# Kernel tuning notes

Hardware: AMD Instinct MI355X
Metric: run time of the kernel (lower is better)

Reference implementation:

```python
import jax, jax.numpy as jnp
import numpy as np

VOCAB = 10000
HID = 1024
OUT = 10000
BATCH = 32
SEQ = 256


def setup_inputs() -> dict:
    key = jax.random.key(0)
    k1, k2, k3, k4 = jax.random.split(key, 4)
    inputs = jax.random.randint(k1, (BATCH, SEQ), 0, VOCAB, dtype=jnp.int32)
    state = jnp.zeros((BATCH, HID), dtype=jnp.float32)
    W_xh = 0.01 * jax.random.normal(k2, (VOCAB, HID), dtype=jnp.float32)
    W_hh = 0.01 * jax.random.normal(k3, (HID, HID), dtype=jnp.float32)
    W_hq = 0.01 * jax.random.normal(k4, (HID, OUT), dtype=jnp.float32)
    b_h = jnp.zeros((HID,), dtype=jnp.float32)
    b_q = jnp.zeros((OUT,), dtype=jnp.float32)
    return {"inputs": inputs, "state": state, "W_xh": W_xh, "W_hh": W_hh,
            "b_h": b_h, "W_hq": W_hq, "b_q": b_q}


def reference(inputs, state, W_xh, W_hh, b_h, W_hq, b_q):
    # inputs: (B, T) int ids. Original one-hots then matmuls with W_xh;
    # one_hot(x) @ W_xh == W_xh[x], so we use the gather form (same math).
    x_tb = inputs.T  # (T, B)

    def step(H, x_t):
        # x_t: (B,) ids; H: (B, HID)
        H = jnp.tanh(W_xh[x_t] + H @ W_hh + b_h)
        Y = H @ W_hq + b_q  # (B, OUT)
        return H, Y

    H_final, Ys = jax.lax.scan(step, state, x_tb)  # Ys: (T, B, OUT)
    # torch.cat(outputs, dim=0) over the time list -> (T*B, OUT)
    Y = Ys.reshape(-1, Ys.shape[-1])
    return Y, H_final
```

## Files before the change

### kernel.cpp

```cpp
#include <hip/hip_runtime.h>
#include <hip/hip_bf16.h>

#define VOCAB 10000
#define HID   1024
#define OUTN  10000
#define BATCH 32
#define SEQT  256
#define NPAD  10112

typedef short s16x8 __attribute__((ext_vector_type(8)));
typedef float f32x4 __attribute__((ext_vector_type(4)));
typedef unsigned u32x2 __attribute__((ext_vector_type(2)));

#define GLOAD_LDS16(gptr, lptr)                                                      \
  __builtin_amdgcn_global_load_lds((__attribute__((address_space(1))) void*)(gptr),  \
                                   (__attribute__((address_space(3))) void*)(lptr),  \
                                   16, 0, 0)

#define ALOAD16_SC(dst, base, off)                                                   \
  asm volatile("global_load_dwordx4 %0, %1, off offset:%2 sc0 sc1"                   \
               : "=v"(dst) : "v"(base), "n"(off) : "memory")

__device__ __forceinline__ unsigned bfbits(float f) {
  __hip_bfloat16 h = __float2bfloat16(f);
  return (unsigned)*reinterpret_cast<unsigned short*>(&h);
}

__global__ __launch_bounds__(256) void transpose_cast(
    const float* __restrict__ src, __hip_bfloat16* __restrict__ dst,
    int K, int N, int Npad) {
  __shared__ float tile[32][33];
  const int n0 = blockIdx.x * 32, k0 = blockIdx.y * 32;
  const int tx = threadIdx.x & 31, ty = threadIdx.x >> 5;
#pragma unroll
  for (int yy = 0; yy < 32; yy += 8) {
    const int k = k0 + ty + yy, n = n0 + tx;
    tile[ty + yy][tx] = (k < K && n < N) ? src[k * N + n] : 0.f;
  }
  __syncthreads();
#pragma unroll
  for (int yy = 0; yy < 32; yy += 8) {
    const int n = n0 + ty + yy, k = k0 + tx;
    if (n < Npad && k < K) dst[(size_t)n * K + k] = __float2bfloat16(tile[tx][ty + yy]);
  }
}

__global__ __launch_bounds__(256) void cast_state(
    const float* __restrict__ s, __hip_bfloat16* __restrict__ d, int n) {
  const int i = blockIdx.x * 256 + threadIdx.x;
  if (i < n) d[i] = __float2bfloat16(s[i]);
}

__global__ __launch_bounds__(256, 1) void rnn_persist(
    __hip_bfloat16* __restrict__ Hbf,
    const int* __restrict__ ids,
    const float* __restrict__ W_xh,
    const __hip_bfloat16* __restrict__ WhhT,
    const float* __restrict__ b_h,
    float* __restrict__ Hfin,
    unsigned* __restrict__ flags) {
  __shared__ __align__(16) __hip_bfloat16 whh[32 * HID];

  const int wg   = blockIdx.x;
  const int wave = threadIdx.x >> 6;
  const int lane = threadIdx.x & 63;
  const int wm = wave >> 1, wn = wave & 1;
  const int r0 = wm * 16;
  const int c0 = wg * 32 + wn * 16;
  const int l16 = lane & 15;
  const int g   = lane >> 4;

  for (int ci = threadIdx.x; ci < 32 * (HID / 8); ci += 256) {
    const int col = ci >> 7;
    const int c16 = ci & 127;
    const s16x8 v = *reinterpret_cast<const s16x8*>(
        WhhT + (size_t)(wg * 32 + col) * HID + c16 * 8);
    const int sw = (c16 & ~7) | ((c16 & 7) ^ (col & 7));
    *reinterpret_cast<s16x8*>(reinterpret_cast<char*>(whh) + col * 2048 + sw * 16) = v;
  }

  const int orow = r0 + l16;
  const int oc   = c0 + g * 4;
  const f32x4 bh4 = *reinterpret_cast<const f32x4*>(b_h + oc);

  f32x4 wxh4 = *reinterpret_cast<const f32x4*>(
      W_xh + (size_t)ids[orow * SEQT + 0] * HID + oc);

  __syncthreads();

  const int aOff = (r0 + l16) * HID + g * 8;
  const char* myB = reinterpret_cast<const char*>(whh) + (wn * 16 + l16) * 2048;
  const int xorv = l16 & 7;
  const int offE = (g ^ xorv) * 16;
  const int offO = ((g + 4) ^ xorv) * 16;

  for (int t = 0; t < SEQT; ++t) {
    const __hip_bfloat16* aBase = Hbf + (size_t)t * (BATCH * HID) + aOff;
    __hip_bfloat16* Hnext = Hbf + (size_t)(t + 1) * (BATCH * HID);

    s16x8 areg[32];
#pragma unroll
    for (int kk = 0; kk < 32; ++kk) ALOAD16_SC(areg[kk], aBase, kk * 64);
    asm volatile("s_waitcnt vmcnt(0)" ::: "memory");
    __builtin_amdgcn_sched_barrier(0);

    f32x4 acc0 = {0.f, 0.f, 0.f, 0.f}, acc1 = {0.f, 0.f, 0.f, 0.f};
#pragma unroll
    for (int kk = 0; kk < 32; kk += 2) {
      const s16x8 b0 = *reinterpret_cast<const s16x8*>(myB + (kk >> 1) * 128 + offE);
      const s16x8 b1 = *reinterpret_cast<const s16x8*>(myB + (kk >> 1) * 128 + offO);
      acc0 = __builtin_amdgcn_mfma_f32_16x16x32_bf16(b0, areg[kk],     acc0, 0, 0, 0);
      acc1 = __builtin_amdgcn_mfma_f32_16x16x32_bf16(b1, areg[kk + 1], acc1, 0, 0, 0);
    }

    float x[4];
#pragma unroll
    for (int jj = 0; jj < 4; ++jj) {
      const float s = acc0[jj] + acc1[jj] + wxh4[jj] + bh4[jj];
      const float e = __expf(2.f * s);
      x[jj] = 1.f - 2.f / (e + 1.f);
    }
    u32x2 pk;
    pk[0] = bfbits(x[0]) | (bfbits(x[1]) << 16);
    pk[1] = bfbits(x[2]) | (bfbits(x[3]) << 16);
    asm volatile("global_store_dwordx2 %0, %1, off sc0 sc1"
                 :: "v"(Hnext + orow * HID + oc), "v"(pk) : "memory");
    if (t == SEQT - 1)
      *reinterpret_cast<f32x4*>(Hfin + orow * HID + oc) = (f32x4){x[0], x[1], x[2], x[3]};

    if (t + 1 < SEQT) {
      asm volatile("s_waitcnt vmcnt(0)" ::: "memory");
      __syncthreads();
      if (threadIdx.x == 0) atomicExch(flags + wg * 32, (unsigned)(t + 1));

      wxh4 = *reinterpret_cast<const f32x4*>(
          W_xh + (size_t)ids[orow * SEQT + (t + 1)] * HID + oc);

      const unsigned* myflag = flags + (lane & 31) * 32;
      const unsigned target = (unsigned)(t + 1);
      unsigned f;
      do {
        asm volatile("global_load_dword %0, %1, off sc0 sc1\n\t"
                     "s_waitcnt vmcnt(0)"
                     : "=v"(f) : "v"(myflag) : "memory");
      } while (__all((int)(f >= target)) == 0);
      __builtin_amdgcn_sched_barrier(0);
    }
  }
}

__global__ __launch_bounds__(256) void gemm_out(
    const __hip_bfloat16* __restrict__ A,
    const __hip_bfloat16* __restrict__ BT,
    const float* __restrict__ b_q,
    float* __restrict__ Y) {
  __shared__ __align__(16) __hip_bfloat16 As[128 * 64];
  __shared__ __align__(16) __hip_bfloat16 Bs[128 * 64];

  const int bx = blockIdx.x;
  const int by = blockIdx.y;
  const int wave = threadIdx.x >> 6;
  const int lane = threadIdx.x & 63;
  const int wm = wave >> 1, wn = wave & 1;
  const int l16 = lane & 15;

  const size_t aRow0 = (size_t)by * 128;
  const size_t bRow0 = (size_t)bx * 128;

  f32x4 acc[4][4];
#pragma unroll
  for (int m = 0; m < 4; ++m)
#pragma unroll
    for (int n = 0; n < 4; ++n) acc[m][n] = (f32x4){0.f, 0.f, 0.f, 0.f};

  for (int kt = 0; kt < HID / 64; ++kt) {
    __syncthreads();
#pragma unroll
    for (int q = 0; q < 4; ++q) {
      const int ci = q * 256 + wave * 64 + lane;
      const int r  = ci >> 3;
      const int gc = (ci & 7) ^ (r & 7);
      const __hip_bfloat16* ga = A  + (aRow0 + r) * HID + kt * 64 + gc * 8;
      const __hip_bfloat16* gb = BT + (bRow0 + r) * HID + kt * 64 + gc * 8;
      GLOAD_LDS16(ga, &As[(q * 256 + wave * 64) * 8]);
      GLOAD_LDS16(gb, &Bs[(q * 256 + wave * 64) * 8]);
    }
    __syncthreads();

    s16x8 af[2][4], bf[2][4];
#pragma unroll
    for (int kc = 0; kc < 2; ++kc) {
      const int cc = kc * 4 + (lane >> 4);
#pragma unroll
      for (int m = 0; m < 4; ++m) {
        const int rowA = wm * 64 + m * 16 + l16;
        af[kc][m] = *reinterpret_cast<const s16x8*>(&As[rowA * 64 + ((cc ^ (rowA & 7)) * 8)]);
      }
#pragma unroll
      for (int n = 0; n < 4; ++n) {
        const int rowB = wn * 64 + n * 16 + l16;
        bf[kc][n] = *reinterpret_cast<const s16x8*>(&Bs[rowB * 64 + ((cc ^ (rowB & 7)) * 8)]);
      }
    }
#pragma unroll
    for (int kc = 0; kc < 2; ++kc)
#pragma unroll
      for (int m = 0; m < 4; ++m)
#pragma unroll
        for (int n = 0; n < 4; ++n)
          acc[m][n] = __builtin_amdgcn_mfma_f32_16x16x32_bf16(af[kc][m], bf[kc][n], acc[m][n], 0, 0, 0);
  }

  const int crow0 = by * 128 + wm * 64 + (lane >> 4) * 4;
  const int ccol0 = bx * 128 + wn * 64 + l16;
#pragma unroll
  for (int n = 0; n < 4; ++n) {
    const int ccol = ccol0 + n * 16;
    if (ccol < OUTN) {
      const float bq = b_q[ccol];
#pragma unroll
      for (int m = 0; m < 4; ++m) {
        const int crow = crow0 + m * 16;
#pragma unroll
        for (int j = 0; j < 4; ++j)
          Y[(size_t)(crow + j) * OUTN + ccol] = acc[m][n][j] + bq;
      }
    }
  }
}

extern "C" void kernel_launch(void* const* d_in, const int* in_sizes, int n_in,
                              void* d_out, int out_size, void* d_ws, size_t ws_size,
                              hipStream_t stream) {
  const int*   inputs = (const int*)d_in[0];
  const float* state  = (const float*)d_in[1];
  const float* W_xh   = (const float*)d_in[2];
  const float* W_hh   = (const float*)d_in[3];
  const float* b_h    = (const float*)d_in[4];
  const float* W_hq   = (const float*)d_in[5];
  const float* b_q    = (const float*)d_in[6];

  float* Y    = (float*)d_out;
  float* Hfin = Y + (size_t)SEQT * BATCH * OUTN;

  char* ws = (char*)d_ws;
  __hip_bfloat16* Hbf  = (__hip_bfloat16*)ws;
  __hip_bfloat16* WhhT = (__hip_bfloat16*)(ws + 16842752);
  __hip_bfloat16* WhqT = (__hip_bfloat16*)(ws + 16842752 + 2097152);
  unsigned* flags      = (unsigned*)(ws + 16842752 + 2097152 + 20709376 - 4096);

  transpose_cast<<<dim3(32, 32), 256, 0, stream>>>(W_hh, WhhT, HID, HID, HID);
  transpose_cast<<<dim3(NPAD / 32, 32), 256, 0, stream>>>(W_hq, WhqT, HID, OUTN, NPAD);
  cast_state<<<dim3(BATCH * HID / 256), 256, 0, stream>>>(state, Hbf, BATCH * HID);

  rnn_persist<<<dim3(32), dim3(256), 0, stream>>>(
      Hbf, inputs, W_xh, WhhT, b_h, Hfin, flags);

  gemm_out<<<dim3(NPAD / 128, 8192 / 128), 256, 0, stream>>>(Hbf + BATCH * HID, WhqT, b_q, Y);
}
```

Before: 1.764 ms.

## Fuse output projection into persistent RNN kernel via flag-synchronized consumer blocks

Adds consumer workgroups to the persistent recurrence kernel that wait on per-step mirror flags and compute Y for each timestep while the recurrence continues, replacing the separate output GEMM launch. Consumers read W_hq fragments straight from global memory without LDS staging. Flags are now zeroed each launch in the state-cast kernel. This risks extra memory traffic and polling contention slowing the latency-critical recurrence.

```diff
diff --git a/kernel.cpp b/kernel.cpp
--- a/kernel.cpp
+++ b/kernel.cpp
@@ -12,11 +12,6 @@
 typedef float f32x4 __attribute__((ext_vector_type(4)));
 typedef unsigned u32x2 __attribute__((ext_vector_type(2)));
 
-#define GLOAD_LDS16(gptr, lptr)                                                      \
-  __builtin_amdgcn_global_load_lds((__attribute__((address_space(1))) void*)(gptr),  \
-                                   (__attribute__((address_space(3))) void*)(lptr),  \
-                                   16, 0, 0)
-
 #define ALOAD16_SC(dst, base, off)                                                   \
   asm volatile("global_load_dwordx4 %0, %1, off offset:%2 sc0 sc1"                   \
                : "=v"(dst) : "v"(base), "n"(off) : "memory")
@@ -46,9 +41,11 @@
 }
 
 __global__ __launch_bounds__(256) void cast_state(
-    const float* __restrict__ s, __hip_bfloat16* __restrict__ d, int n) {
+    const float* __restrict__ s, __hip_bfloat16* __restrict__ d, int n,
+    unsigned* __restrict__ zero_base, int zero_n) {
   const int i = blockIdx.x * 256 + threadIdx.x;
   if (i < n) d[i] = __float2bfloat16(s[i]);
+  if (i < zero_n) zero_base[i] = 0u;
 }
 
 __global__ __launch_bounds__(256, 1) void rnn_persist(
@@ -58,172 +55,165 @@
     const __hip_bfloat16* __restrict__ WhhT,
     const float* __restrict__ b_h,
     float* __restrict__ Hfin,
-    unsigned* __restrict__ flags) {
-  __shared__ __align__(16) __hip_bfloat16 whh[32 * HID];
-
-  const int wg   = blockIdx.x;
-  const int wave = threadIdx.x >> 6;
-  const int lane = threadIdx.x & 63;
-  const int wm = wave >> 1, wn = wave & 1;
-  const int r0 = wm * 16;
-  const int c0 = wg * 32 + wn * 16;
-  const int l16 = lane & 15;
-  const int g   = lane >> 4;
-
-  for (int ci = threadIdx.x; ci < 32 * (HID / 8); ci += 256) {
-    const int col = ci >> 7;
-    const int c16 = ci & 127;
-    const s16x8 v = *reinterpret_cast<const s16x8*>(
-        WhhT + (size_t)(wg * 32 + col) * HID + c16 * 8);
-    const int sw = (c16 & ~7) | ((c16 & 7) ^ (col & 7));
-    *reinterpret_cast<s16x8*>(reinterpret_cast<char*>(whh) + col * 2048 + sw * 16) = v;
-  }
-
-  const int orow = r0 + l16;
-  const int oc   = c0 + g * 4;
-  const f32x4 bh4 = *reinterpret_cast<const f32x4*>(b_h + oc);
-
-  f32x4 wxh4 = *reinterpret_cast<const f32x4*>(
-      W_xh + (size_t)ids[orow * SEQT + 0] * HID + oc);
-
-  __syncthreads();
-
-  const int aOff = (r0 + l16) * HID + g * 8;
-  const char* myB = reinterpret_cast<const char*>(whh) + (wn * 16 + l16) * 2048;
-  const int xorv = l16 & 7;
-  const int offE = (g ^ xorv) * 16;
-  const int offO = ((g + 4) ^ xorv) * 16;
-
-  for (int t = 0; t < SEQT; ++t) {
-    const __hip_bfloat16* aBase = Hbf + (size_t)t * (BATCH * HID) + aOff;
-    __hip_bfloat16* Hnext = Hbf + (size_t)(t + 1) * (BATCH * HID);
-
-    s16x8 areg[32];
-#pragma unroll
-    for (int kk = 0; kk < 32; ++kk) ALOAD16_SC(areg[kk], aBase, kk * 64);
-    asm volatile("s_waitcnt vmcnt(0)" ::: "memory");
-    __builtin_amdgcn_sched_barrier(0);
-
-    f32x4 acc0 = {0.f, 0.f, 0.f, 0.f}, acc1 = {0.f, 0.f, 0.f, 0.f};
-#pragma unroll
-    for (int kk = 0; kk < 32; kk += 2) {
-      const s16x8 b0 = *reinterpret_cast<const s16x8*>(myB + (kk >> 1) * 128 + offE);
-      const s16x8 b1 = *reinterpret_cast<const s16x8*>(myB + (kk >> 1) * 128 + offO);
-      acc0 = __builtin_amdgcn_mfma_f32_16x16x32_bf16(b0, areg[kk],     acc0, 0, 0, 0);
-      acc1 = __builtin_amdgcn_mfma_f32_16x16x32_bf16(b1, areg[kk + 1], acc1, 0, 0, 0);
-    }
-
-    float x[4];
-#pragma unroll
-    for (int jj = 0; jj < 4; ++jj) {
-      const float s = acc0[jj] + acc1[jj] + wxh4[jj] + bh4[jj];
-      const float e = __expf(2.f * s);
-      x[jj] = 1.f - 2.f / (e + 1.f);
-    }
-    u32x2 pk;
-    pk[0] = bfbits(x[0]) | (bfbits(x[1]) << 16);
-    pk[1] = bfbits(x[2]) | (bfbits(x[3]) << 16);
-    asm volatile("global_store_dwordx2 %0, %1, off sc0 sc1"
-                 :: "v"(Hnext + orow * HID + oc), "v"(pk) : "memory");
-    if (t == SEQT - 1)
-      *reinterpret_cast<f32x4*>(Hfin + orow * HID + oc) = (f32x4){x[0], x[1], x[2], x[3]};
-
-    if (t + 1 < SEQT) {
-      asm volatile("s_waitcnt vmcnt(0)" ::: "memory");
-      __syncthreads();
-      if (threadIdx.x == 0) atomicExch(flags + wg * 32, (unsigned)(t + 1));
-
-      wxh4 = *reinterpret_cast<const f32x4*>(
-          W_xh + (size_t)ids[orow * SEQT + (t + 1)] * HID + oc);
-
-      const unsigned* myflag = flags + (lane & 31) * 32;
-      const unsigned target = (unsigned)(t + 1);
-      unsigned f;
-      do {
-        asm volatile("global_load_dword %0, %1, off sc0 sc1\n\t"
-                     "s_waitcnt vmcnt(0)"
-                     : "=v"(f) : "v"(myflag) : "memory");
-      } while (__all((int)(f >= target)) == 0);
-      __builtin_amdgcn_sched_barrier(0);
-    }
-  }
-}
-
-__global__ __launch_bounds__(256) void gemm_out(
-    const __hip_bfloat16* __restrict__ A,
-    const __hip_bfloat16* __restrict__ BT,
+    unsigned* __restrict__ flags,
+    unsigned* __restrict__ mirror,
+    const __hip_bfloat16* __restrict__ WhqT,
     const float* __restrict__ b_q,
     float* __restrict__ Y) {
-  __shared__ __align__(16) __hip_bfloat16 As[128 * 64];
-  __shared__ __align__(16) __hip_bfloat16 Bs[128 * 64];
-
-  const int bx = blockIdx.x;
-  const int by = blockIdx.y;
+  __shared__ __align__(16) __hip_bfloat16 whh[32 * HID];
+
   const int wave = threadIdx.x >> 6;
   const int lane = threadIdx.x & 63;
   const int wm = wave >> 1, wn = wave & 1;
   const int l16 = lane & 15;
-
-  const size_t aRow0 = (size_t)by * 128;
-  const size_t bRow0 = (size_t)bx * 128;
-
-  f32x4 acc[4][4];
-#pragma unroll
-  for (int m = 0; m < 4; ++m)
-#pragma unroll
-    for (int n = 0; n < 4; ++n) acc[m][n] = (f32x4){0.f, 0.f, 0.f, 0.f};
-
-  for (int kt = 0; kt < HID / 64; ++kt) {
+  const int g   = lane >> 4;
+
+  if (blockIdx.x < 32) {
+    const int wg = blockIdx.x;
+    const int r0 = wm * 16;
+    const int c0 = wg * 32 + wn * 16;
+
+    for (int ci = threadIdx.x; ci < 32 * (HID / 8); ci += 256) {
+      const int col = ci >> 7;
+      const int c16 = ci & 127;
+      const s16x8 v = *reinterpret_cast<const s16x8*>(
+          WhhT + (size_t)(wg * 32 + col) * HID + c16 * 8);
+      const int sw = (c16 & ~7) | ((c16 & 7) ^ (col & 7));
+      *reinterpret_cast<s16x8*>(reinterpret_cast<char*>(whh) + col * 2048 + sw * 16) = v;
+    }
+
+    const int orow = r0 + l16;
+    const int oc   = c0 + g * 4;
+    const f32x4 bh4 = *reinterpret_cast<const f32x4*>(b_h + oc);
+
+    f32x4 wxh4 = *reinterpret_cast<const f32x4*>(
+        W_xh + (size_t)ids[orow * SEQT + 0] * HID + oc);
+
     __syncthreads();
-#pragma unroll
-    for (int q = 0; q < 4; ++q) {
-      const int ci = q * 256 + wave * 64 + lane;
-      const int r  = ci >> 3;
-      const int gc = (ci & 7) ^ (r & 7);
-      const __hip_bfloat16* ga = A  + (aRow0 + r) * HID + kt * 64 + gc * 8;
-      const __hip_bfloat16* gb = BT + (bRow0 + r) * HID + kt * 64 + gc * 8;
-      GLOAD_LDS16(ga, &As[(q * 256 + wave * 64) * 8]);
-      GLOAD_LDS16(gb, &Bs[(q * 256 + wave * 64) * 8]);
-    }
+
+    const int aOff = (r0 + l16) * HID + g * 8;
+    const char* myB = reinterpret_cast<const char*>(whh) + (wn * 16 + l16) * 2048;
+    const int xorv = l16 & 7;
+    const int offE = (g ^ xorv) * 16;
+    const int offO = ((g + 4) ^ xorv) * 16;
+
+    for (int t = 0; t < SEQT; ++t) {
+      const __hip_bfloat16* aBase = Hbf + (size_t)t * (BATCH * HID) + aOff;
+      __hip_bfloat16* Hnext = Hbf + (size_t)(t + 1) * (BATCH * HID);
+
+      s16x8 areg[32];
+#pragma unroll
+      for (int kk = 0; kk < 32; ++kk) ALOAD16_SC(areg[kk], aBase, kk * 64);
+      asm volatile("s_waitcnt vmcnt(0)" ::: "memory");
+      __builtin_amdgcn_sched_barrier(0);
+
+      f32x4 acc0 = {0.f, 0.f, 0.f, 0.f}, acc1 = {0.f, 0.f, 0.f, 0.f};
+#pragma unroll
+      for (int kk = 0; kk < 32; kk += 2) {
+        const s16x8 b0 = *reinterpret_cast<const s16x8*>(myB + (kk >> 1) * 128 + offE);
+        const s16x8 b1 = *reinterpret_cast<const s16x8*>(myB + (kk >> 1) * 128 + offO);
+        acc0 = __builtin_amdgcn_mfma_f32_16x16x32_bf16(b0, areg[kk],     acc0, 0, 0, 0);
+        acc1 = __builtin_amdgcn_mfma_f32_16x16x32_bf16(b1, areg[kk + 1], acc1, 0, 0, 0);
+      }
+
+      float x[4];
+#pragma unroll
+      for (int jj = 0; jj < 4; ++jj) {
+        const float s = acc0[jj] + acc1[jj] + wxh4[jj] + bh4[jj];
+        const float e = __expf(2.f * s);
+        x[jj] = 1.f - 2.f / (e + 1.f);
+      }
+      u32x2 pk;
+      pk[0] = bfbits(x[0]) | (bfbits(x[1]) << 16);
+      pk[1] = bfbits(x[2]) | (bfbits(x[3]) << 16);
+      asm volatile("global_store_dwordx2 %0, %1, off sc0 sc1"
+                   :: "v"(Hnext + orow * HID + oc), "v"(pk) : "memory");
+      if (t == SEQT - 1)
+        *reinterpret_cast<f32x4*>(Hfin + orow * HID + oc) = (f32x4){x[0], x[1], x[2], x[3]};
+
+      if (t + 1 < SEQT) {
+        asm volatile("s_waitcnt vmcnt(0)" ::: "memory");
+        __syncthreads();
+        if (threadIdx.x == 0) {
+          atomicExch(flags + wg * 32, (unsigned)(t + 1));
+          atomicExch(mirror + wg * 32, (unsigned)(t + 1));
+        }
+
+        wxh4 = *reinterpret_cast<const f32x4*>(
+            W_xh + (size_t)ids[orow * SEQT + (t + 1)] * HID + oc);
+
+        const unsigned* myflag = flags + (lane & 31) * 32;
+        const unsigned target = (unsigned)(t + 1);
+        unsigned f;
+        do {
+          asm volatile("global_load_dword %0, %1, off sc0 sc1\n\t"
+                       "s_waitcnt vmcnt(0)"
+                       : "=v"(f) : "v"(myflag) : "memory");
+        } while (__all((int)(f >= target)) == 0);
+        __builtin_amdgcn_sched_barrier(0);
+      }
+    }
+    asm volatile("s_waitcnt vmcnt(0)" ::: "memory");
     __syncthreads();
-
-    s16x8 af[2][4], bf[2][4];
-#pragma unroll
-    for (int kc = 0; kc < 2; ++kc) {
-      const int cc = kc * 4 + (lane >> 4);
-#pragma unroll
-      for (int m = 0; m < 4; ++m) {
-        const int rowA = wm * 64 + m * 16 + l16;
-        af[kc][m] = *reinterpret_cast<const s16x8*>(&As[rowA * 64 + ((cc ^ (rowA & 7)) * 8)]);
-      }
+    if (threadIdx.x == 0) {
+      atomicExch(flags + blockIdx.x * 32, (unsigned)SEQT);
+      atomicExch(mirror + blockIdx.x * 32, (unsigned)SEQT);
+    }
+    return;
+  }
+
+  const int cw = blockIdx.x - 32;
+  const int yr0 = wm * 16 + g * 4;
+
+  const __hip_bfloat16* wq[4];
+  float bq[4];
+  int ocol[4];
+#pragma unroll
+  for (int n = 0; n < 4; ++n) {
+    ocol[n] = cw * 128 + wn * 64 + n * 16 + l16;
+    wq[n] = WhqT + (size_t)ocol[n] * HID + g * 8;
+    bq[n] = (ocol[n] < OUTN) ? b_q[ocol[n]] : 0.f;
+  }
+  const int aOff = (wm * 16 + l16) * HID + g * 8;
+
+  for (int tt = 1; tt <= SEQT; ++tt) {
+    {
+      const unsigned* myflag = mirror + (lane & 31) * 32;
+      unsigned f;
+      while (true) {
+        asm volatile("global_load_dword %0, %1, off sc0 sc1\n\t"
+                     "s_waitcnt vmcnt(0)"
+                     : "=v"(f) : "v"(myflag) : "memory");
+        if (__all((int)(f >= (unsigned)tt))) break;
+        __builtin_amdgcn_s_sleep(8);
+      }
+      __builtin_amdgcn_sched_barrier(0);
+    }
+
+    s16x8 areg[32];
+    const __hip_bfloat16* aBase = Hbf + (size_t)tt * (BATCH * HID) + aOff;
+#pragma unroll
+    for (int kk = 0; kk < 32; ++kk) ALOAD16_SC(areg[kk], aBase, kk * 64);
+    asm volatile("s_waitcnt vmcnt(0)" ::: "memory");
+    __builtin_amdgcn_sched_barrier(0);
+
+    f32x4 acc[4] = {{0.f,0.f,0.f,0.f},{0.f,0.f,0.f,0.f},{0.f,0.f,0.f,0.f},{0.f,0.f,0.f,0.f}};
+#pragma unroll
+    for (int kk = 0; kk < 32; ++kk) {
 #pragma unroll
       for (int n = 0; n < 4; ++n) {
-        const int rowB = wn * 64 + n * 16 + l16;
-        bf[kc][n] = *reinterpret_cast<const s16x8*>(&Bs[rowB * 64 + ((cc ^ (rowB & 7)) * 8)]);
-      }
-    }
-#pragma unroll
-    for (int kc = 0; kc < 2; ++kc)
-#pragma unroll
-      for (int m = 0; m < 4; ++m)
-#pragma unroll
-        for (int n = 0; n < 4; ++n)
-          acc[m][n] = __builtin_amdgcn_mfma_f32_16x16x32_bf16(af[kc][m], bf[kc][n], acc[m][n], 0, 0, 0);
-  }
-
-  const int crow0 = by * 128 + wm * 64 + (lane >> 4) * 4;
-  const int ccol0 = bx * 128 + wn * 64 + l16;
-#pragma unroll
-  for (int n = 0; n < 4; ++n) {
-    const int ccol = ccol0 + n * 16;
-    if (ccol < OUTN) {
-      const float bq = b_q[ccol];
-#pragma unroll
-      for (int m = 0; m < 4; ++m) {
-        const int crow = crow0 + m * 16;
+        const s16x8 w = *reinterpret_cast<const s16x8*>(wq[n] + kk * 32);
+        acc[n] = __builtin_amdgcn_mfma_f32_16x16x32_bf16(areg[kk], w, acc[n], 0, 0, 0);
+      }
+    }
+
+    const size_t yrBase = (size_t)(tt - 1) * 32 + yr0;
+#pragma unroll
+    for (int n = 0; n < 4; ++n) {
+      if (ocol[n] < OUTN) {
 #pragma unroll
         for (int j = 0; j < 4; ++j)
-          Y[(size_t)(crow + j) * OUTN + ccol] = acc[m][n][j] + bq;
+          Y[(yrBase + j) * OUTN + ocol[n]] = acc[n][j] + bq[n];
       }
     }
   }
@@ -246,15 +236,15 @@
   char* ws = (char*)d_ws;
   __hip_bfloat16* Hbf  = (__hip_bfloat16*)ws;
   __hip_bfloat16* WhhT = (__hip_bfloat16*)(ws + 16842752);
-  __hip_bfloat16* WhqT = (__hip_bfloat16*)(ws + 16842752 + 2097152);
-  unsigned* flags      = (unsigned*)(ws + 16842752 + 2097152 + 20709376 - 4096);
+  __hip_bfloat16* WhqT = (__hip_bfloat16*)(ws + 18939904);
+  unsigned* flags      = (unsigned*)(ws + 39649280);
+  unsigned* mirror     = (unsigned*)(ws + 39653376);
+  const int zero_n = 8192 / 4;
 
   transpose_cast<<<dim3(32, 32), 256, 0, stream>>>(W_hh, WhhT, HID, HID, HID);
   transpose_cast<<<dim3(NPAD / 32, 32), 256, 0, stream>>>(W_hq, WhqT, HID, OUTN, NPAD);
-  cast_state<<<dim3(BATCH * HID / 256), 256, 0, stream>>>(state, Hbf, BATCH * HID);
-
-  rnn_persist<<<dim3(32), dim3(256), 0, stream>>>(
-      Hbf, inputs, W_xh, WhhT, b_h, Hfin, flags);
-
-  gemm_out<<<dim3(NPAD / 128, 8192 / 128), 256, 0, stream>>>(Hbf + BATCH * HID, WhqT, b_q, Y);
-}
+  cast_state<<<dim3(128), 256, 0, stream>>>(state, Hbf, BATCH * HID, flags, zero_n);
+
+  rnn_persist<<<dim3(32 + NPAD / 128), dim3(256), 0, stream>>>(
+      Hbf, inputs, W_xh, WhhT, b_h, Hfin, flags, mirror, WhqT, b_q, Y);
+}
```

New measurement: 4.617 ms. 162% more time.

## Fuse output GEMM into persistent RNN kernel, overlapping it with the recurrence via flags

Applied to the files above, without the earlier changes.

The output projection GEMM now runs in extra workgroups (79 of them) launched alongside the 32 recurrent workgroups in a single persistent kernel. Each GEMM workgroup owns one N-tile and walks all 64 M-tiles in order, polling a mirror flag array until the recurrent blocks have published the four timesteps that tile needs. This overlaps the GEMM with the serial recurrence instead of running it afterwards. In exchange, each GEMM workgroup processes its 64 tiles one after another, and the spin-polling plus co-residency needs (all 111 blocks must be resident, or the kernel can deadlock) add contention and risk. The flags are now also zeroed inside cast_state.

```diff
diff --git a/kernel.cpp b/kernel.cpp
--- a/kernel.cpp
+++ b/kernel.cpp
@@ -46,9 +46,11 @@
 }
 
 __global__ __launch_bounds__(256) void cast_state(
-    const float* __restrict__ s, __hip_bfloat16* __restrict__ d, int n) {
+    const float* __restrict__ s, __hip_bfloat16* __restrict__ d, int n,
+    unsigned* __restrict__ zero_base, int zero_n) {
   const int i = blockIdx.x * 256 + threadIdx.x;
   if (i < n) d[i] = __float2bfloat16(s[i]);
+  if (i < zero_n) zero_base[i] = 0u;
 }
 
 __global__ __launch_bounds__(256, 1) void rnn_persist(
@@ -58,172 +60,194 @@
     const __hip_bfloat16* __restrict__ WhhT,
     const float* __restrict__ b_h,
     float* __restrict__ Hfin,
-    unsigned* __restrict__ flags) {
-  __shared__ __align__(16) __hip_bfloat16 whh[32 * HID];
-
-  const int wg   = blockIdx.x;
-  const int wave = threadIdx.x >> 6;
-  const int lane = threadIdx.x & 63;
-  const int wm = wave >> 1, wn = wave & 1;
-  const int r0 = wm * 16;
-  const int c0 = wg * 32 + wn * 16;
-  const int l16 = lane & 15;
-  const int g   = lane >> 4;
-
-  for (int ci = threadIdx.x; ci < 32 * (HID / 8); ci += 256) {
-    const int col = ci >> 7;
-    const int c16 = ci & 127;
-    const s16x8 v = *reinterpret_cast<const s16x8*>(
-        WhhT + (size_t)(wg * 32 + col) * HID + c16 * 8);
-    const int sw = (c16 & ~7) | ((c16 & 7) ^ (col & 7));
-    *reinterpret_cast<s16x8*>(reinterpret_cast<char*>(whh) + col * 2048 + sw * 16) = v;
-  }
-
-  const int orow = r0 + l16;
-  const int oc   = c0 + g * 4;
-  const f32x4 bh4 = *reinterpret_cast<const f32x4*>(b_h + oc);
-
-  f32x4 wxh4 = *reinterpret_cast<const f32x4*>(
-      W_xh + (size_t)ids[orow * SEQT + 0] * HID + oc);
-
-  __syncthreads();
-
-  const int aOff = (r0 + l16) * HID + g * 8;
-  const char* myB = reinterpret_cast<const char*>(whh) + (wn * 16 + l16) * 2048;
-  const int xorv = l16 & 7;
-  const int offE = (g ^ xorv) * 16;
-  const int offO = ((g + 4) ^ xorv) * 16;
-
-  for (int t = 0; t < SEQT; ++t) {
-    const __hip_bfloat16* aBase = Hbf + (size_t)t * (BATCH * HID) + aOff;
-    __hip_bfloat16* Hnext = Hbf + (size_t)(t + 1) * (BATCH * HID);
-
-    s16x8 areg[32];
-#pragma unroll
-    for (int kk = 0; kk < 32; ++kk) ALOAD16_SC(areg[kk], aBase, kk * 64);
-    asm volatile("s_waitcnt vmcnt(0)" ::: "memory");
-    __builtin_amdgcn_sched_barrier(0);
-
-    f32x4 acc0 = {0.f, 0.f, 0.f, 0.f}, acc1 = {0.f, 0.f, 0.f, 0.f};
-#pragma unroll
-    for (int kk = 0; kk < 32; kk += 2) {
-      const s16x8 b0 = *reinterpret_cast<const s16x8*>(myB + (kk >> 1) * 128 + offE);
-      const s16x8 b1 = *reinterpret_cast<const s16x8*>(myB + (kk >> 1) * 128 + offO);
-      acc0 = __builtin_amdgcn_mfma_f32_16x16x32_bf16(b0, areg[kk],     acc0, 0, 0, 0);
-      acc1 = __builtin_amdgcn_mfma_f32_16x16x32_bf16(b1, areg[kk + 1], acc1, 0, 0, 0);
-    }
-
-    float x[4];
-#pragma unroll
-    for (int jj = 0; jj < 4; ++jj) {
-      const float s = acc0[jj] + acc1[jj] + wxh4[jj] + bh4[jj];
-      const float e = __expf(2.f * s);
-      x[jj] = 1.f - 2.f / (e + 1.f);
-    }
-    u32x2 pk;
-    pk[0] = bfbits(x[0]) | (bfbits(x[1]) << 16);
-    pk[1] = bfbits(x[2]) | (bfbits(x[3]) << 16);
-    asm volatile("global_store_dwordx2 %0, %1, off sc0 sc1"
-                 :: "v"(Hnext + orow * HID + oc), "v"(pk) : "memory");
-    if (t == SEQT - 1)
-      *reinterpret_cast<f32x4*>(Hfin + orow * HID + oc) = (f32x4){x[0], x[1], x[2], x[3]};
-
-    if (t + 1 < SEQT) {
-      asm volatile("s_waitcnt vmcnt(0)" ::: "memory");
-      __syncthreads();
-      if (threadIdx.x == 0) atomicExch(flags + wg * 32, (unsigned)(t + 1));
-
-      wxh4 = *reinterpret_cast<const f32x4*>(
-          W_xh + (size_t)ids[orow * SEQT + (t + 1)] * HID + oc);
-
-      const unsigned* myflag = flags + (lane & 31) * 32;
-      const unsigned target = (unsigned)(t + 1);
-      unsigned f;
-      do {
-        asm volatile("global_load_dword %0, %1, off sc0 sc1\n\t"
-                     "s_waitcnt vmcnt(0)"
-                     : "=v"(f) : "v"(myflag) : "memory");
-      } while (__all((int)(f >= target)) == 0);
-      __builtin_amdgcn_sched_barrier(0);
-    }
-  }
-}
-
-__global__ __launch_bounds__(256) void gemm_out(
-    const __hip_bfloat16* __restrict__ A,
-    const __hip_bfloat16* __restrict__ BT,
+    unsigned* __restrict__ flags,
+    unsigned* __restrict__ mirror,
+    const __hip_bfloat16* __restrict__ WhqT,
     const float* __restrict__ b_q,
     float* __restrict__ Y) {
-  __shared__ __align__(16) __hip_bfloat16 As[128 * 64];
-  __shared__ __align__(16) __hip_bfloat16 Bs[128 * 64];
-
-  const int bx = blockIdx.x;
-  const int by = blockIdx.y;
+  __shared__ __align__(16) __hip_bfloat16 smem[32 * HID];
+
   const int wave = threadIdx.x >> 6;
   const int lane = threadIdx.x & 63;
   const int wm = wave >> 1, wn = wave & 1;
   const int l16 = lane & 15;
-
-  const size_t aRow0 = (size_t)by * 128;
+  const int g   = lane >> 4;
+
+  if (blockIdx.x < 32) {
+    __hip_bfloat16* whh = smem;
+    const int wg = blockIdx.x;
+    const int r0 = wm * 16;
+    const int c0 = wg * 32 + wn * 16;
+
+    for (int ci = threadIdx.x; ci < 32 * (HID / 8); ci += 256) {
+      const int col = ci >> 7;
+      const int c16 = ci & 127;
+      const s16x8 v = *reinterpret_cast<const s16x8*>(
+          WhhT + (size_t)(wg * 32 + col) * HID + c16 * 8);
+      const int sw = (c16 & ~7) | ((c16 & 7) ^ (col & 7));
+      *reinterpret_cast<s16x8*>(reinterpret_cast<char*>(whh) + col * 2048 + sw * 16) = v;
+    }
+
+    const int orow = r0 + l16;
+    const int oc   = c0 + g * 4;
+    const f32x4 bh4 = *reinterpret_cast<const f32x4*>(b_h + oc);
+
+    f32x4 wxh4 = *reinterpret_cast<const f32x4*>(
+        W_xh + (size_t)ids[orow * SEQT + 0] * HID + oc);
+
+    __syncthreads();
+
+    const int aOff = (r0 + l16) * HID + g * 8;
+    const char* myB = reinterpret_cast<const char*>(whh) + (wn * 16 + l16) * 2048;
+    const int xorv = l16 & 7;
+    const int offE = (g ^ xorv) * 16;
+    const int offO = ((g + 4) ^ xorv) * 16;
+
+    for (int t = 0; t < SEQT; ++t) {
+      const __hip_bfloat16* aBase = Hbf + (size_t)t * (BATCH * HID) + aOff;
+      __hip_bfloat16* Hnext = Hbf + (size_t)(t + 1) * (BATCH * HID);
+
+      s16x8 areg[32];
+#pragma unroll
+      for (int kk = 0; kk < 32; ++kk) ALOAD16_SC(areg[kk], aBase, kk * 64);
+      asm volatile("s_waitcnt vmcnt(0)" ::: "memory");
+      __builtin_amdgcn_sched_barrier(0);
+
+      f32x4 acc0 = {0.f, 0.f, 0.f, 0.f}, acc1 = {0.f, 0.f, 0.f, 0.f};
+#pragma unroll
+      for (int kk = 0; kk < 32; kk += 2) {
+        const s16x8 b0 = *reinterpret_cast<const s16x8*>(myB + (kk >> 1) * 128 + offE);
+        const s16x8 b1 = *reinterpret_cast<const s16x8*>(myB + (kk >> 1) * 128 + offO);
+        acc0 = __builtin_amdgcn_mfma_f32_16x16x32_bf16(b0, areg[kk],     acc0, 0, 0, 0);
+        acc1 = __builtin_amdgcn_mfma_f32_16x16x32_bf16(b1, areg[kk + 1], acc1, 0, 0, 0);
+      }
+
+      float x[4];
+#pragma unroll
+      for (int jj = 0; jj < 4; ++jj) {
+        const float s = acc0[jj] + acc1[jj] + wxh4[jj] + bh4[jj];
+        const float e = __expf(2.f * s);
+        x[jj] = 1.f - 2.f / (e + 1.f);
+      }
+      u32x2 pk;
+      pk[0] = bfbits(x[0]) | (bfbits(x[1]) << 16);
+      pk[1] = bfbits(x[2]) | (bfbits(x[3]) << 16);
+      asm volatile("global_store_dwordx2 %0, %1, off sc0 sc1"
+                   :: "v"(Hnext + orow * HID + oc), "v"(pk) : "memory");
+      if (t == SEQT - 1)
+        *reinterpret_cast<f32x4*>(Hfin + orow * HID + oc) = (f32x4){x[0], x[1], x[2], x[3]};
+
+      if (t + 1 < SEQT) {
+        asm volatile("s_waitcnt vmcnt(0)" ::: "memory");
+        __syncthreads();
+        if (threadIdx.x == 0) {
+          atomicExch(flags + wg * 32, (unsigned)(t + 1));
+          atomicExch(mirror + wg * 32, (unsigned)(t + 1));
+        }
+
+        wxh4 = *reinterpret_cast<const f32x4*>(
+            W_xh + (size_t)ids[orow * SEQT + (t + 1)] * HID + oc);
+
+        const unsigned* myflag = flags + (lane & 31) * 32;
+        const unsigned target = (unsigned)(t + 1);
+        unsigned f;
+        do {
+          asm volatile("global_load_dword %0, %1, off sc0 sc1\n\t"
+                       "s_waitcnt vmcnt(0)"
+                       : "=v"(f) : "v"(myflag) : "memory");
+        } while (__all((int)(f >= target)) == 0);
+        __builtin_amdgcn_sched_barrier(0);
+      }
+    }
+    asm volatile("s_waitcnt vmcnt(0)" ::: "memory");
+    __syncthreads();
+    if (threadIdx.x == 0) {
+      atomicExch(flags + blockIdx.x * 32, (unsigned)SEQT);
+      atomicExch(mirror + blockIdx.x * 32, (unsigned)SEQT);
+    }
+    return;
+  }
+
+  __hip_bfloat16* As = smem;
+  __hip_bfloat16* Bs = smem + 128 * 64;
+  const int bx = blockIdx.x - 32;
+  const __hip_bfloat16* A = Hbf + BATCH * HID;
   const size_t bRow0 = (size_t)bx * 128;
 
-  f32x4 acc[4][4];
-#pragma unroll
-  for (int m = 0; m < 4; ++m)
-#pragma unroll
-    for (int n = 0; n < 4; ++n) acc[m][n] = (f32x4){0.f, 0.f, 0.f, 0.f};
-
-  for (int kt = 0; kt < HID / 64; ++kt) {
-    __syncthreads();
-#pragma unroll
-    for (int q = 0; q < 4; ++q) {
-      const int ci = q * 256 + wave * 64 + lane;
-      const int r  = ci >> 3;
-      const int gc = (ci & 7) ^ (r & 7);
-      const __hip_bfloat16* ga = A  + (aRow0 + r) * HID + kt * 64 + gc * 8;
-      const __hip_bfloat16* gb = BT + (bRow0 + r) * HID + kt * 64 + gc * 8;
-      GLOAD_LDS16(ga, &As[(q * 256 + wave * 64) * 8]);
-      GLOAD_LDS16(gb, &Bs[(q * 256 + wave * 64) * 8]);
-    }
-    __syncthreads();
-
-    s16x8 af[2][4], bf[2][4];
-#pragma unroll
-    for (int kc = 0; kc < 2; ++kc) {
-      const int cc = kc * 4 + (lane >> 4);
-#pragma unroll
-      for (int m = 0; m < 4; ++m) {
-        const int rowA = wm * 64 + m * 16 + l16;
-        af[kc][m] = *reinterpret_cast<const s16x8*>(&As[rowA * 64 + ((cc ^ (rowA & 7)) * 8)]);
-      }
-#pragma unroll
-      for (int n = 0; n < 4; ++n) {
-        const int rowB = wn * 64 + n * 16 + l16;
-        bf[kc][n] = *reinterpret_cast<const s16x8*>(&Bs[rowB * 64 + ((cc ^ (rowB & 7)) * 8)]);
-      }
-    }
-#pragma unroll
-    for (int kc = 0; kc < 2; ++kc)
-#pragma unroll
-      for (int m = 0; m < 4; ++m)
-#pragma unroll
-        for (int n = 0; n < 4; ++n)
-          acc[m][n] = __builtin_amdgcn_mfma_f32_16x16x32_bf16(af[kc][m], bf[kc][n], acc[m][n], 0, 0, 0);
-  }
-
-  const int crow0 = by * 128 + wm * 64 + (lane >> 4) * 4;
-  const int ccol0 = bx * 128 + wn * 64 + l16;
-#pragma unroll
-  for (int n = 0; n < 4; ++n) {
-    const int ccol = ccol0 + n * 16;
-    if (ccol < OUTN) {
-      const float bq = b_q[ccol];
-#pragma unroll
-      for (int m = 0; m < 4; ++m) {
-        const int crow = crow0 + m * 16;
-#pragma unroll
-        for (int j = 0; j < 4; ++j)
-          Y[(size_t)(crow + j) * OUTN + ccol] = acc[m][n][j] + bq;
+  for (int mt = 0; mt < 64; ++mt) {
+    {
+      const unsigned need = (unsigned)((mt + 1) * 4);
+      const unsigned* myflag = mirror + (lane & 31) * 32;
+      unsigned f;
+      while (true) {
+        asm volatile("global_load_dword %0, %1, off sc0 sc1\n\t"
+                     "s_waitcnt vmcnt(0)"
+                     : "=v"(f) : "v"(myflag) : "memory");
+        if (__all((int)(f >= need))) break;
+        __builtin_amdgcn_s_sleep(8);
+      }
+      __builtin_amdgcn_sched_barrier(0);
+    }
+
+    const size_t aRow0 = (size_t)mt * 128;
+    f32x4 acc[4][4];
+#pragma unroll
+    for (int m = 0; m < 4; ++m)
+#pragma unroll
+      for (int n = 0; n < 4; ++n) acc[m][n] = (f32x4){0.f, 0.f, 0.f, 0.f};
+
+    for (int kt = 0; kt < HID / 64; ++kt) {
+      __syncthreads();
+#pragma unroll
+      for (int q = 0; q < 4; ++q) {
+        const int ci = q * 256 + wave * 64 + lane;
+        const int r  = ci >> 3;
+        const int gc = (ci & 7) ^ (r & 7);
+        const __hip_bfloat16* ga = A    + (aRow0 + r) * HID + kt * 64 + gc * 8;
+        const __hip_bfloat16* gb = WhqT + (bRow0 + r) * HID + kt * 64 + gc * 8;
+        GLOAD_LDS16(ga, &As[(q * 256 + wave * 64) * 8]);
+        GLOAD_LDS16(gb, &Bs[(q * 256 + wave * 64) * 8]);
+      }
+      __syncthreads();
+
+      s16x8 af[2][4], bf[2][4];
+#pragma unroll
+      for (int kc = 0; kc < 2; ++kc) {
+        const int cc = kc * 4 + g;
+#pragma unroll
+        for (int m = 0; m < 4; ++m) {
+          const int rowA = wm * 64 + m * 16 + l16;
+          af[kc][m] = *reinterpret_cast<const s16x8*>(&As[rowA * 64 + ((cc ^ (rowA & 7)) * 8)]);
+        }
+#pragma unroll
+        for (int n = 0; n < 4; ++n) {
+          const int rowB = wn * 64 + n * 16 + l16;
+          bf[kc][n] = *reinterpret_cast<const s16x8*>(&Bs[rowB * 64 + ((cc ^ (rowB & 7)) * 8)]);
+        }
+      }
+#pragma unroll
+      for (int kc = 0; kc < 2; ++kc)
+#pragma unroll
+        for (int m = 0; m < 4; ++m)
+#pragma unroll
+          for (int n = 0; n < 4; ++n)
+            acc[m][n] = __builtin_amdgcn_mfma_f32_16x16x32_bf16(af[kc][m], bf[kc][n], acc[m][n], 0, 0, 0);
+    }
+
+    const int crow0 = (int)aRow0 + wm * 64 + g * 4;
+    const int ccol0 = bx * 128 + wn * 64 + l16;
+#pragma unroll
+    for (int n = 0; n < 4; ++n) {
+      const int ccol = ccol0 + n * 16;
+      if (ccol < OUTN) {
+        const float bq = b_q[ccol];
+#pragma unroll
+        for (int m = 0; m < 4; ++m) {
+          const int crow = crow0 + m * 16;
+#pragma unroll
+          for (int j = 0; j < 4; ++j)
+            Y[(size_t)(crow + j) * OUTN + ccol] = acc[m][n][j] + bq;
+        }
       }
     }
   }
@@ -246,15 +270,15 @@
   char* ws = (char*)d_ws;
   __hip_bfloat16* Hbf  = (__hip_bfloat16*)ws;
   __hip_bfloat16* WhhT = (__hip_bfloat16*)(ws + 16842752);
-  __hip_bfloat16* WhqT = (__hip_bfloat16*)(ws + 16842752 + 2097152);
-  unsigned* flags      = (unsigned*)(ws + 16842752 + 2097152 + 20709376 - 4096);
+  __hip_bfloat16* WhqT = (__hip_bfloat16*)(ws + 18939904);
+  unsigned* flags      = (unsigned*)(ws + 39649280);
+  unsigned* mirror     = (unsigned*)(ws + 39653376);
+  const int zero_n = 8192 / 4;
 
   transpose_cast<<<dim3(32, 32), 256, 0, stream>>>(W_hh, WhhT, HID, HID, HID);
   transpose_cast<<<dim3(NPAD / 32, 32), 256, 0, stream>>>(W_hq, WhqT, HID, OUTN, NPAD);
-  cast_state<<<dim3(BATCH * HID / 256), 256, 0, stream>>>(state, Hbf, BATCH * HID);
-
-  rnn_persist<<<dim3(32), dim3(256), 0, stream>>>(
-      Hbf, inputs, W_xh, WhhT, b_h, Hfin, flags);
-
-  gemm_out<<<dim3(NPAD / 128, 8192 / 128), 256, 0, stream>>>(Hbf + BATCH * HID, WhqT, b_q, Y);
-}
+  cast_state<<<dim3(128), 256, 0, stream>>>(state, Hbf, BATCH * HID, flags, zero_n);
+
+  rnn_persist<<<dim3(32 + NPAD / 128), dim3(256), 0, stream>>>(
+      Hbf, inputs, W_xh, WhhT, b_h, Hfin, flags, mirror, WhqT, b_q, Y);
+}
```

Result: faster. 1.560 ms (median of 2 runs) (-11.5%).
